# Kernel optimization log

Hardware: AMD Instinct MI355X
Metric: run time of the kernel (lower is better)

The kernel has to match this reference:

```python
import jax, jax.numpy as jnp
import numpy as np

# TT factorization of a 4096 -> 4096 linear layer
IN_SHAPE = (8, 8, 8, 8)    # input_tt_shape, prod = 4096
OUT_SHAPE = (8, 8, 8, 8)   # output_tt_shape, prod = 4096
RANKS = (1, 16, 16, 16, 1) # tt_ranks, len = n_dim + 1
N_DIM = len(IN_SHAPE)
BATCH = 2048
OUT_SIZE = int(np.prod(OUT_SHAPE))
IN_SIZE = int(np.prod(IN_SHAPE))


def setup_inputs() -> dict:
    key = jax.random.key(0)
    ks = jax.random.split(key, N_DIM + 1)
    x = jax.random.normal(ks[0], (BATCH, IN_SIZE), dtype=jnp.float32)
    inp = {"x": x}
    for i in range(N_DIM):
        rows = RANKS[i] * OUT_SHAPE[i]
        cols = IN_SHAPE[i] * RANKS[i + 1]
        # xavier_uniform scale, matching torch init statistics
        limit = float(np.sqrt(6.0 / (rows + cols)))
        inp[f"core{i}"] = jax.random.uniform(
            ks[i + 1], (rows, cols), minval=-limit, maxval=limit, dtype=jnp.float32
        )
    inp["bias"] = jnp.zeros((OUT_SIZE,), dtype=jnp.float32)
    return inp


def reference(x, core0, core1, core2, core3, bias):
    cores = [core0, core1, core2, core3]
    res = x  # [B, prod(IN_SHAPE)]
    # Sequential TT-core contraction, last mode first (faithful to torch loop)
    for k in range(N_DIM - 1, -1, -1):
        res = res.reshape(-1, IN_SHAPE[k])                     # [.., n_k]
        res = res.T                                            # [n_k, ..]
        res = res.reshape(RANKS[k + 1] * IN_SHAPE[k], -1)      # [r_{k+1}*n_k, ..]
        res = cores[k] @ res                                   # [r_k*m_k, ..]
    res = res.reshape(OUT_SIZE, -1).T                          # [B, prod(OUT_SHAPE)]
    return res + bias
```

## Files before the change

### kernel.cpp

```cpp
#include <hip/hip_runtime.h>
#include <hip/hip_bf16.h>
#include <stdint.h>


typedef __bf16 bf16_t;
typedef __bf16 bf16x8 __attribute__((ext_vector_type(8)));
typedef float floatx4 __attribute__((ext_vector_type(4)));

#define BATCH_N 2048
#define KD 4096
#define ND 4096

__device__ static inline void load_lds16(const void* g, void* l) {
    __builtin_amdgcn_global_load_lds(
        (const __attribute__((address_space(1))) void*)g,
        (__attribute__((address_space(3))) void*)l, 16, 0, 0);
}

__global__ __launch_bounds__(256) void cvt_x(const float* __restrict__ x,
                                             bf16_t* __restrict__ xb) {
    int t = blockIdx.x * 256 + threadIdx.x;
    const float4* xv = (const float4*)x;
    float4 a = xv[t * 2];
    float4 b = xv[t * 2 + 1];
    bf16x8 o;
    o[0] = (bf16_t)a.x; o[1] = (bf16_t)a.y; o[2] = (bf16_t)a.z; o[3] = (bf16_t)a.w;
    o[4] = (bf16_t)b.x; o[5] = (bf16_t)b.y; o[6] = (bf16_t)b.z; o[7] = (bf16_t)b.w;
    ((bf16x8*)xb)[t] = o;
}

__global__ __launch_bounds__(256) void build_p(const float* __restrict__ c0,
                                               const float* __restrict__ c1,
                                               float* __restrict__ P) {
    int o = blockIdx.x * 256 + threadIdx.x;
    int r2 = o & 15, N01 = (o >> 4) & 63, M01 = o >> 10;
    int m0 = M01 >> 3, m1 = M01 & 7, n0 = N01 >> 3, n1 = N01 & 7;
    float s = 0.f;
#pragma unroll
    for (int r1 = 0; r1 < 16; ++r1)
        s += c0[m0 * 128 + n0 * 16 + r1] * c1[(r1 * 8 + m1) * 128 + n1 * 16 + r2];
    P[o] = s;
}

__global__ __launch_bounds__(256) void build_t1(const float* __restrict__ c2,
                                                const float* __restrict__ c3,
                                                float* __restrict__ T1) {
    int o = blockIdx.x * 256 + threadIdx.x;
    int N23 = o & 63, M23 = (o >> 6) & 63, r2 = o >> 12;
    int n2 = N23 >> 3, n3 = N23 & 7, m2 = M23 >> 3, m3 = M23 & 7;
    float s = 0.f;
#pragma unroll
    for (int r3 = 0; r3 < 16; ++r3)
        s += c2[(r2 * 8 + m2) * 128 + n2 * 16 + r3] * c3[(r3 * 8 + m3) * 8 + n3];
    T1[o] = s;
}

__global__ __launch_bounds__(256) void build_w(const float* __restrict__ P,
                                               const float* __restrict__ T1,
                                               bf16_t* __restrict__ W) {
    __shared__ float Pl[64 * 16];
    __shared__ float T1l[16 * 64];
    int b = blockIdx.x;
    int M23 = b >> 6, N01 = b & 63;
    int t = threadIdx.x;
    for (int i = t; i < 1024; i += 256) {
        int m01 = i >> 4, r2 = i & 15;
        Pl[i] = P[m01 * 1024 + N01 * 16 + r2];
    }
    for (int i = t; i < 1024; i += 256) {
        int r2 = i >> 6, n23 = i & 63;
        T1l[i] = T1[r2 * 4096 + M23 * 64 + n23];
    }
    __syncthreads();
    int n23 = t & 63, q = t >> 6;
#pragma unroll
    for (int g = 0; g < 16; ++g) {
        int m01 = q * 16 + g;
        float s = 0.f;
#pragma unroll
        for (int r2 = 0; r2 < 16; ++r2) s += Pl[m01 * 16 + r2] * T1l[r2 * 64 + n23];
        W[(size_t)(m01 * 64 + M23) * 4096 + N01 * 64 + n23] = (bf16_t)s;
    }
}

__global__ __launch_bounds__(256) void gemm_bt(const bf16_t* __restrict__ A,
                                               const bf16_t* __restrict__ B,
                                               const float* __restrict__ bias,
                                               float* __restrict__ C) {
    __shared__ bf16_t As[128 * 32];
    __shared__ bf16_t Bs[128 * 32];
    const int t = threadIdx.x;
    const int bn = blockIdx.x, bm = blockIdx.y;
    const int lane = t & 63, wave = t >> 6;
    const int wm = wave >> 1, wn = wave & 1;

    const int sr = t >> 2;
    const int sk = (t & 3) * 8;
    const bf16_t* Agp = A + (size_t)(bm * 128 + sr) * KD + sk;
    const bf16_t* Bgp = B + (size_t)(bn * 128 + sr) * KD + sk;

    floatx4 acc[4][4];
    floatx4 zero = {0.f, 0.f, 0.f, 0.f};
#pragma unroll
    for (int i = 0; i < 4; ++i)
#pragma unroll
        for (int j = 0; j < 4; ++j) acc[i][j] = zero;

    const int fr = lane & 15;
    const int fk = (lane >> 4) * 8;

    for (int k0 = 0; k0 < KD; k0 += 32) {
        __syncthreads();
#pragma unroll
        for (int h = 0; h < 2; ++h) {
            load_lds16(Agp + (size_t)(h * 64) * KD + k0, As + h * 2048 + wave * 512);
            load_lds16(Bgp + (size_t)(h * 64) * KD + k0, Bs + h * 2048 + wave * 512);
        }
        __syncthreads();

        bf16x8 af[4], bf[4];
#pragma unroll
        for (int im = 0; im < 4; ++im)
            af[im] = *(const bf16x8*)(As + (wm * 64 + im * 16 + fr) * 32 + fk);
#pragma unroll
        for (int in = 0; in < 4; ++in)
            bf[in] = *(const bf16x8*)(Bs + (wn * 64 + in * 16 + fr) * 32 + fk);
#pragma unroll
        for (int im = 0; im < 4; ++im)
#pragma unroll
            for (int in = 0; in < 4; ++in)
                acc[im][in] = __builtin_amdgcn_mfma_f32_16x16x32_bf16(
                    af[im], bf[in], acc[im][in], 0, 0, 0);
    }

    const int rl = lane >> 4, cl = lane & 15;
    const size_t rbase = (size_t)bm * 128 + wm * 64;
    const int cbase = bn * 128 + wn * 64;
#pragma unroll
    for (int im = 0; im < 4; ++im) {
#pragma unroll
        for (int in = 0; in < 4; ++in) {
            int col = cbase + in * 16 + cl;
            float bv = bias[col];
#pragma unroll
            for (int r = 0; r < 4; ++r) {
                size_t row = rbase + im * 16 + rl * 4 + r;
                C[row * ND + col] = acc[im][in][r] + bv;
            }
        }
    }
}

extern "C" void kernel_launch(void* const* d_in, const int* in_sizes, int n_in,
                              void* d_out, int out_size, void* d_ws, size_t ws_size,
                              hipStream_t stream) {
    const float* x  = (const float*)d_in[0];
    const float* c0 = (const float*)d_in[1];
    const float* c1 = (const float*)d_in[2];
    const float* c2 = (const float*)d_in[3];
    const float* c3 = (const float*)d_in[4];
    const float* bias = (const float*)d_in[5];
    float* out = (float*)d_out;

    char* ws = (char*)d_ws;
    bf16_t* Xb = (bf16_t*)ws;
    bf16_t* W  = (bf16_t*)(ws + (16u << 20));
    float*  P  = (float*)(ws + (48u << 20));
    float*  T1 = (float*)(ws + (48u << 20) + (256u << 10));

    cvt_x<<<4096, 256, 0, stream>>>(x, Xb);
    build_p<<<256, 256, 0, stream>>>(c0, c1, P);
    build_t1<<<256, 256, 0, stream>>>(c2, c3, T1);
    build_w<<<4096, 256, 0, stream>>>(P, T1, W);
    dim3 grid(ND / 128, BATCH_N / 128);
    gemm_bt<<<grid, 256, 0, stream>>>(Xb, W, bias, out);
}
```

Baseline: 196.9 us.

## Fuse TT core builders into build_w, shrink GEMM M-tile and swizzle LDS

Merges the P and T1 precompute kernels into build_w, so each block computes its slices from the TT cores staged in shared memory. This removes two launches and the intermediate global buffers. The GEMM tile is halved in M to 64 rows, doubling the grid for better CU fill, and the LDS k-chunk layout is XOR-swizzled to reduce bank conflicts on fragment reads. The costs are redundant per-block recompute of the core products and lower data reuse per GEMM tile.

```diff
diff --git a/kernel.cpp b/kernel.cpp
--- a/kernel.cpp
+++ b/kernel.cpp
@@ -29,56 +29,59 @@
     ((bf16x8*)xb)[t] = o;
 }
 
-__global__ __launch_bounds__(256) void build_p(const float* __restrict__ c0,
+__global__ __launch_bounds__(256) void build_w(const float* __restrict__ c0,
                                                const float* __restrict__ c1,
-                                               float* __restrict__ P) {
-    int o = blockIdx.x * 256 + threadIdx.x;
-    int r2 = o & 15, N01 = (o >> 4) & 63, M01 = o >> 10;
-    int m0 = M01 >> 3, m1 = M01 & 7, n0 = N01 >> 3, n1 = N01 & 7;
-    float s = 0.f;
+                                               const float* __restrict__ c2,
+                                               const float* __restrict__ c3,
+                                               bf16_t* __restrict__ W) {
+    __shared__ float c0s[8 * 16];
+    __shared__ float c1s[16 * 8 * 16];
+    __shared__ float c2s[16 * 8 * 16];
+    __shared__ float c3s[16 * 8];
+    __shared__ float Ps[64 * 16];
+    __shared__ float T1s[16 * 64];
+    const int b = blockIdx.x;
+    const int M23 = b >> 6, N01 = b & 63;
+    const int n0 = N01 >> 3, n1 = N01 & 7, m2 = M23 >> 3, m3 = M23 & 7;
+    const int t = threadIdx.x;
+
+    if (t < 128) c0s[t] = c0[(t >> 4) * 128 + n0 * 16 + (t & 15)];
+    if (t < 128) c3s[t] = c3[((t >> 3) * 8 + m3) * 8 + (t & 7)];
+    for (int i = t; i < 2048; i += 256) {
+        int r1 = i >> 7, m1 = (i >> 4) & 7, r2 = i & 15;
+        c1s[i] = c1[(r1 * 8 + m1) * 128 + n1 * 16 + r2];
+    }
+    for (int i = t; i < 2048; i += 256) {
+        int r2 = i >> 7, n2 = (i >> 4) & 7, r3 = i & 15;
+        c2s[i] = c2[(r2 * 8 + m2) * 128 + n2 * 16 + r3];
+    }
+    __syncthreads();
+
+    for (int i = t; i < 1024; i += 256) {
+        int m01 = i >> 4, r2 = i & 15, m0 = m01 >> 3, m1 = m01 & 7;
+        float s = 0.f;
 #pragma unroll
-    for (int r1 = 0; r1 < 16; ++r1)
-        s += c0[m0 * 128 + n0 * 16 + r1] * c1[(r1 * 8 + m1) * 128 + n1 * 16 + r2];
-    P[o] = s;
-}
-
-__global__ __launch_bounds__(256) void build_t1(const float* __restrict__ c2,
-                                                const float* __restrict__ c3,
-                                                float* __restrict__ T1) {
-    int o = blockIdx.x * 256 + threadIdx.x;
-    int N23 = o & 63, M23 = (o >> 6) & 63, r2 = o >> 12;
-    int n2 = N23 >> 3, n3 = N23 & 7, m2 = M23 >> 3, m3 = M23 & 7;
-    float s = 0.f;
-#pragma unroll
-    for (int r3 = 0; r3 < 16; ++r3)
-        s += c2[(r2 * 8 + m2) * 128 + n2 * 16 + r3] * c3[(r3 * 8 + m3) * 8 + n3];
-    T1[o] = s;
-}
-
-__global__ __launch_bounds__(256) void build_w(const float* __restrict__ P,
-                                               const float* __restrict__ T1,
-                                               bf16_t* __restrict__ W) {
-    __shared__ float Pl[64 * 16];
-    __shared__ float T1l[16 * 64];
-    int b = blockIdx.x;
-    int M23 = b >> 6, N01 = b & 63;
-    int t = threadIdx.x;
-    for (int i = t; i < 1024; i += 256) {
-        int m01 = i >> 4, r2 = i & 15;
-        Pl[i] = P[m01 * 1024 + N01 * 16 + r2];
+        for (int r1 = 0; r1 < 16; ++r1)
+            s += c0s[m0 * 16 + r1] * c1s[r1 * 128 + m1 * 16 + r2];
+        Ps[i] = s;
     }
     for (int i = t; i < 1024; i += 256) {
-        int r2 = i >> 6, n23 = i & 63;
-        T1l[i] = T1[r2 * 4096 + M23 * 64 + n23];
+        int r2 = i >> 6, n23 = i & 63, n2 = n23 >> 3, n3 = n23 & 7;
+        float s = 0.f;
+#pragma unroll
+        for (int r3 = 0; r3 < 16; ++r3)
+            s += c2s[r2 * 128 + n2 * 16 + r3] * c3s[r3 * 8 + n3];
+        T1s[i] = s;
     }
     __syncthreads();
-    int n23 = t & 63, q = t >> 6;
+
+    const int n23 = t & 63, q = t >> 6;
 #pragma unroll
     for (int g = 0; g < 16; ++g) {
         int m01 = q * 16 + g;
         float s = 0.f;
 #pragma unroll
-        for (int r2 = 0; r2 < 16; ++r2) s += Pl[m01 * 16 + r2] * T1l[r2 * 64 + n23];
+        for (int r2 = 0; r2 < 16; ++r2) s += Ps[m01 * 16 + r2] * T1s[r2 * 64 + n23];
         W[(size_t)(m01 * 64 + M23) * 4096 + N01 * 64 + n23] = (bf16_t)s;
     }
 }
@@ -87,7 +90,7 @@
                                                const bf16_t* __restrict__ B,
                                                const float* __restrict__ bias,
                                                float* __restrict__ C) {
-    __shared__ bf16_t As[128 * 32];
+    __shared__ bf16_t As[64 * 32];
     __shared__ bf16_t Bs[128 * 32];
     const int t = threadIdx.x;
     const int bn = blockIdx.x, bm = blockIdx.y;
@@ -95,38 +98,39 @@
     const int wm = wave >> 1, wn = wave & 1;
 
     const int sr = t >> 2;
-    const int sk = (t & 3) * 8;
-    const bf16_t* Agp = A + (size_t)(bm * 128 + sr) * KD + sk;
+    const int sk = ((t & 3) ^ ((t >> 3) & 3)) * 8;
+    const bf16_t* Agp = A + (size_t)(bm * 64 + sr) * KD + sk;
     const bf16_t* Bgp = B + (size_t)(bn * 128 + sr) * KD + sk;
+    bf16_t* AsW = As + wave * 512;
+    bf16_t* BsW0 = Bs + wave * 512;
+    bf16_t* BsW1 = Bs + 2048 + wave * 512;
 
-    floatx4 acc[4][4];
+    floatx4 acc[2][4];
     floatx4 zero = {0.f, 0.f, 0.f, 0.f};
 #pragma unroll
-    for (int i = 0; i < 4; ++i)
+    for (int i = 0; i < 2; ++i)
 #pragma unroll
         for (int j = 0; j < 4; ++j) acc[i][j] = zero;
 
     const int fr = lane & 15;
-    const int fk = (lane >> 4) * 8;
+    const int pk = ((lane >> 4) ^ ((lane >> 1) & 3)) * 8;
 
     for (int k0 = 0; k0 < KD; k0 += 32) {
         __syncthreads();
-#pragma unroll
-        for (int h = 0; h < 2; ++h) {
-            load_lds16(Agp + (size_t)(h * 64) * KD + k0, As + h * 2048 + wave * 512);
-            load_lds16(Bgp + (size_t)(h * 64) * KD + k0, Bs + h * 2048 + wave * 512);
-        }
+        load_lds16(Agp + k0, AsW);
+        load_lds16(Bgp + k0, BsW0);
+        load_lds16(Bgp + (size_t)64 * KD + k0, BsW1);
         __syncthreads();
 
-        bf16x8 af[4], bf[4];
+        bf16x8 af[2], bf[4];
 #pragma unroll
-        for (int im = 0; im < 4; ++im)
-            af[im] = *(const bf16x8*)(As + (wm * 64 + im * 16 + fr) * 32 + fk);
+        for (int im = 0; im < 2; ++im)
+            af[im] = *(const bf16x8*)(As + (wm * 32 + im * 16 + fr) * 32 + pk);
 #pragma unroll
         for (int in = 0; in < 4; ++in)
-            bf[in] = *(const bf16x8*)(Bs + (wn * 64 + in * 16 + fr) * 32 + fk);
+            bf[in] = *(const bf16x8*)(Bs + (wn * 64 + in * 16 + fr) * 32 + pk);
 #pragma unroll
-        for (int im = 0; im < 4; ++im)
+        for (int im = 0; im < 2; ++im)
 #pragma unroll
             for (int in = 0; in < 4; ++in)
                 acc[im][in] = __builtin_amdgcn_mfma_f32_16x16x32_bf16(
@@ -134,10 +138,10 @@
     }
 
     const int rl = lane >> 4, cl = lane & 15;
-    const size_t rbase = (size_t)bm * 128 + wm * 64;
+    const size_t rbase = (size_t)bm * 64 + wm * 32;
     const int cbase = bn * 128 + wn * 64;
 #pragma unroll
-    for (int im = 0; im < 4; ++im) {
+    for (int im = 0; im < 2; ++im) {
 #pragma unroll
         for (int in = 0; in < 4; ++in) {
             int col = cbase + in * 16 + cl;
@@ -165,13 +169,9 @@
     char* ws = (char*)d_ws;
     bf16_t* Xb = (bf16_t*)ws;
     bf16_t* W  = (bf16_t*)(ws + (16u << 20));
-    float*  P  = (float*)(ws + (48u << 20));
-    float*  T1 = (float*)(ws + (48u << 20) + (256u << 10));
 
     cvt_x<<<4096, 256, 0, stream>>>(x, Xb);
-    build_p<<<256, 256, 0, stream>>>(c0, c1, P);
-    build_t1<<<256, 256, 0, stream>>>(c2, c3, T1);
-    build_w<<<4096, 256, 0, stream>>>(P, T1, W);
-    dim3 grid(ND / 128, BATCH_N / 128);
+    build_w<<<4096, 256, 0, stream>>>(c0, c1, c2, c3, W);
+    dim3 grid(ND / 128, BATCH_N / 64);
     gemm_bt<<<grid, 256, 0, stream>>>(Xb, W, bias, out);
 }
```

Measured after the change: 210.8 us. 7.1% more time.
